# Performance work log

Hardware: AMD Instinct MI355X
Metric: run time of the kernel (lower is better)

Reference implementation:

```python
import jax, jax.numpy as jnp
import numpy as np

B, T, D_IN = 8192, 12, 64   # trajectories, traj length (== max_length), input dim
HID, ENC, R = 512, 128, 64  # encoder hidden, encoded_dim, MPS rank
OUT = 1


def _uniform(key, shape, bound):
    return jax.random.uniform(key, shape, jnp.float32, -bound, bound)


def setup_inputs() -> dict:
    key = jax.random.key(0)
    ks = jax.random.split(key, 8)
    x = jax.random.normal(ks[0], (B, T, D_IN), jnp.float32)
    # encoder Linear params (Kaiming-uniform-like scale)
    W1 = _uniform(ks[1], (HID, D_IN), 1.0 / np.sqrt(D_IN))
    b1 = _uniform(ks[2], (HID,), 1.0 / np.sqrt(D_IN))
    W2 = _uniform(ks[3], (ENC, HID), 1.0 / np.sqrt(HID))
    b2 = _uniform(ks[4], (ENC,), 1.0 / np.sqrt(HID))
    # MPS cores with if_rescale_weights bound = 1/sqrt(prod(dims))
    H_first = _uniform(ks[5], (1, ENC, R), 1.0 / np.sqrt(1 * ENC * R))
    H_mid = _uniform(ks[6], (T - 2, R, ENC, R), 1.0 / np.sqrt(R * ENC * R))
    H_last = _uniform(ks[7], (R, ENC, OUT), 1.0 / np.sqrt(R * ENC * OUT))
    return {"x": x, "W1": W1, "b1": b1, "W2": W2, "b2": b2,
            "H_first": H_first, "H_mid": H_mid, "H_last": H_last}


def reference(x, W1, b1, W2, b2, H_first, H_mid, H_last):
    Bn, Tn, _ = x.shape
    # two-layer encoder MLP with ReLU after each layer
    h = jax.nn.relu(jnp.einsum('btd,hd->bth', x, W1) + b1)
    enc = jax.nn.relu(jnp.einsum('bth,eh->bte', h, W2) + b2)  # [B, T, ENC]
    # contract each timestep's encoding with its core along the physical dim
    v = jnp.einsum('be,oer->br', enc[:, 0], H_first)              # [B, R] (dim0==1 squeezed)
    M = jnp.einsum('bte,tper->btpr', enc[:, 1:Tn - 1], H_mid)     # [B, T-2, R, R]
    # sequential chain product (vector-matrix, associative scan structure)
    for t in range(Tn - 2):
        v = jnp.einsum('bp,bpr->br', v, M[:, t])
    last = jnp.einsum('be,per->bpr', enc[:, -1], H_last)          # [B, R, OUT]
    out = jnp.einsum('bp,bpo->bo', v, last)                       # [B, OUT]
    return out.squeeze(-1)                                        # [B] (output_dim == 1)
```

## Files before the change

### kernel.cpp

```cpp
#include <hip/hip_runtime.h>
#include <hip/hip_fp16.h>


#define B_ALL 8192
#define TT    12
#define B_T   32
#define NBLK  256

typedef short bfrag __attribute__((ext_vector_type(8)));
typedef _Float16 hfrag __attribute__((ext_vector_type(8)));
typedef float ffrag __attribute__((ext_vector_type(16)));

#define O_ENC   0ULL
#define O_HMH   25165824ULL
#define O_HML   35651584ULL
#define O_W1F   46137344ULL
#define O_W2F   46202880ULL

__device__ __forceinline__ unsigned short bf16_rne(float f) {
    unsigned int u = __builtin_bit_cast(unsigned int, f);
    unsigned int r = (u + 0x7fffu + ((u >> 16) & 1u)) >> 16;
    return (unsigned short)r;
}
__device__ __forceinline__ float bf16_f32(unsigned short h) {
    unsigned int u = ((unsigned int)h) << 16;
    return __builtin_bit_cast(float, u);
}

__global__ __launch_bounds__(256)
void prep_kernel(const float* __restrict__ W1, const float* __restrict__ W2,
                 const float* __restrict__ Hm,
                 __half* __restrict__ w1f, __half* __restrict__ w2f,
                 unsigned short* __restrict__ Hh, unsigned short* __restrict__ Hl)
{
    const long long N_W1 = 32768, N_W2 = 65536, N_H = 10LL * 128 * 4096;
    const long long total = N_W1 + N_W2 + N_H;
    const long long stride = (long long)gridDim.x * blockDim.x;
    for (long long idx = (long long)blockIdx.x * blockDim.x + threadIdx.x;
         idx < total; idx += stride) {
        if (idx < N_W1) {
            const int w = (int)idx;
            const int jn = w >> 11, ks = (w >> 9) & 3, half = (w >> 8) & 1;
            const int jl = (w >> 3) & 31, jj = w & 7;
            const int j = jn * 32 + jl, d = ks * 16 + half * 8 + jj;
            w1f[w] = __float2half(W1[j * 64 + d]);
        } else if (idx < N_W1 + N_W2) {
            const int w = (int)(idx - N_W1);
            const int en = w >> 14, ks2g = (w >> 9) & 31, half = (w >> 8) & 1;
            const int el = (w >> 3) & 31, jj = w & 7;
            const int e = en * 32 + el, j = ks2g * 16 + half * 8 + jj;
            w2f[w] = __float2half(W2[e * 512 + j]);
        } else {
            const long long q = idx - N_W1 - N_W2;
            const int t = (int)(q / 524288);
            const int rem = (int)(q % 524288);
            const int e = rem >> 12;
            const int f = rem & 4095;
            const int mf = f >> 11, s = (f >> 9) & 3, half = (f >> 8) & 1;
            const int l = (f >> 3) & 31, j = f & 7;
            const int p = s * 16 + half * 8 + j;
            const int r = mf * 32 + l;
            const float val = Hm[(((long long)t * 64 + p) * 128 + e) * 64 + r];
            const unsigned short hi = bf16_rne(val);
            const unsigned short lo = bf16_rne(val - bf16_f32(hi));
            Hh[q] = hi;
            Hl[q] = lo;
        }
    }
}

__global__ __launch_bounds__(256)
void enc_kernel(const float* __restrict__ x,
                const float* __restrict__ b1, const float* __restrict__ b2,
                const __half* __restrict__ w1f, const __half* __restrict__ w2f,
                __half* __restrict__ encH)
{
    __shared__ __align__(16) unsigned char smem[17408];
    float* x_s  = (float*)smem;
    __half* h_s = (__half*)smem;

    const int tid   = threadIdx.x;
    const int wv    = tid >> 6;
    const int lane  = tid & 63;
    const int l32   = lane & 31;
    const int half  = lane >> 5;
    const int msub  = wv >> 1;
    const int nhalf = wv & 1;
    const int m0    = blockIdx.x * 64;

    #pragma unroll
    for (int i = 0; i < 4; ++i) {
        const int f4 = i * 256 + tid;
        const int r = f4 >> 4, c4 = (f4 & 15) * 4;
        *(float4*)&x_s[r * 68 + c4] =
            *(const float4*)&x[(long long)(m0 + r) * 64 + c4];
    }
    __syncthreads();

    hfrag xa[4];
    #pragma unroll
    for (int ks = 0; ks < 4; ++ks) {
        const float* src = &x_s[(msub * 32 + l32) * 68 + ks * 16 + half * 8];
        const float4 a = *(const float4*)src;
        const float4 b = *(const float4*)(src + 4);
        hfrag v;
        v[0] = (_Float16)a.x; v[1] = (_Float16)a.y;
        v[2] = (_Float16)a.z; v[3] = (_Float16)a.w;
        v[4] = (_Float16)b.x; v[5] = (_Float16)b.y;
        v[6] = (_Float16)b.z; v[7] = (_Float16)b.w;
        xa[ks] = v;
    }
    __syncthreads();

    ffrag c2[2];
    c2[0] = 0.0f; c2[1] = 0.0f;

    for (int chunk = 0; chunk < 4; ++chunk) {
        ffrag c1[2];
        float b1j[2];
        #pragma unroll
        for (int nf = 0; nf < 2; ++nf) {
            const int jn = chunk * 4 + nhalf * 2 + nf;
            b1j[nf] = b1[jn * 32 + l32];
            ffrag acc = 0.0f;
            #pragma unroll
            for (int ks = 0; ks < 4; ++ks) {
                const hfrag bh = *(const hfrag*)(w1f + (jn * 4 + ks) * 512
                                                 + half * 256 + l32 * 8);
                acc = __builtin_amdgcn_mfma_f32_32x32x16_f16(xa[ks], bh, acc, 0, 0, 0);
            }
            c1[nf] = acc;
        }
        __syncthreads();
        #pragma unroll
        for (int nf = 0; nf < 2; ++nf) {
            #pragma unroll
            for (int i2 = 0; i2 < 16; ++i2) {
                const int m_row = (i2 & 3) + 8 * (i2 >> 2) + 4 * half;
                const float v = fmaxf(c1[nf][i2] + b1j[nf], 0.0f);
                h_s[(msub * 32 + m_row) * 136 + nhalf * 64 + nf * 32 + l32] =
                    __float2half(v);
            }
        }
        __syncthreads();
        #pragma unroll
        for (int ks2 = 0; ks2 < 8; ++ks2) {
            const hfrag a = *(const hfrag*)&h_s[(msub * 32 + l32) * 136
                                                + ks2 * 16 + half * 8];
            const int ks2g = chunk * 8 + ks2;
            #pragma unroll
            for (int ef = 0; ef < 2; ++ef) {
                const int en = nhalf * 2 + ef;
                const hfrag b = *(const hfrag*)(w2f + (en * 32 + ks2g) * 512
                                                + half * 256 + l32 * 8);
                c2[ef] = __builtin_amdgcn_mfma_f32_32x32x16_f16(a, b, c2[ef], 0, 0, 0);
            }
        }
    }

    #pragma unroll
    for (int ef = 0; ef < 2; ++ef) {
        const int e = nhalf * 64 + ef * 32 + l32;
        const float b2e = b2[e];
        #pragma unroll
        for (int i2 = 0; i2 < 16; ++i2) {
            const int m_row = (i2 & 3) + 8 * (i2 >> 2) + 4 * half;
            const int m_g = m0 + msub * 32 + m_row;
            encH[(long long)m_g * 128 + e] =
                __float2half(fmaxf(c2[ef][i2] + b2e, 0.0f));
        }
    }
}

__global__ __launch_bounds__(512, 1)
void chain_all(const unsigned short* __restrict__ HmH,
               const unsigned short* __restrict__ HmL,
               const __half* __restrict__ encH,
               const float* __restrict__ Hf,
               const float* __restrict__ HL,
               float* __restrict__ out)
{
    __shared__ __align__(16) unsigned char smem[60480];
    float* vsum  = (float*)smem;
    float* enc_s = (float*)(smem + 8448);
    float* scr   = (float*)(smem + 25344);
    float* hl_s  = (float*)(smem + 25344);
    float* red   = (float*)(smem + 58368);

    const int tid  = threadIdx.x;
    const int b0   = blockIdx.x * B_T;
    const int lane = tid & 63;
    const int wv   = tid >> 6;
    const int l32  = lane & 31;
    const int half = lane >> 5;
    const int eq   = wv >> 1;
    const int rh   = wv & 1;

    const int sbL = tid >> 4;
    const int seo = (tid & 15) * 8;
    #define STAGE_ENC(T)                                                      \
    {                                                                         \
        const __half* er = encH + ((size_t)(b0 + sbL) * 12 + (T)) * 128 + seo;\
        uint4 u = *(const uint4*)er;                                          \
        const __half* hp = (const __half*)&u;                                 \
        _Pragma("unroll")                                                     \
        for (int j = 0; j < 8; ++j)                                           \
            enc_s[(seo + j) * 33 + sbL] = __half2float(hp[j]);                \
    }

    {
        STAGE_ENC(0);
        __syncthreads();
        const int bI = tid & 31, pg = tid >> 5;
        const int p0 = pg * 4;
        float a0 = 0, a1 = 0, a2 = 0, a3 = 0;
        for (int e = 0; e < 128; ++e) {
            const float ev = enc_s[e * 33 + bI];
            const float4 h = *(const float4*)&Hf[e * 64 + p0];
            a0 += ev * h.x; a1 += ev * h.y; a2 += ev * h.z; a3 += ev * h.w;
        }
        vsum[(p0 + 0) * 33 + bI] = a0;
        vsum[(p0 + 1) * 33 + bI] = a1;
        vsum[(p0 + 2) * 33 + bI] = a2;
        vsum[(p0 + 3) * 33 + bI] = a3;
        __syncthreads();
    }

    const unsigned short* Hsh = HmH;
    const unsigned short* Hsl = HmL;
    const int lanoff = rh * 2048 + half * 256 + l32 * 8;

    #pragma unroll 1
    for (int t = 1; t <= 10; ++t) {
        STAGE_ENC(t);

        bfrag vbh[4], vbl[4];
        #pragma unroll
        for (int s = 0; s < 4; ++s) {
            const int p0 = s * 16 + half * 8;
            bfrag hb, lb;
            #pragma unroll
            for (int j = 0; j < 8; ++j) {
                const float f = vsum[(p0 + j) * 33 + l32];
                const unsigned short hi = bf16_rne(f);
                const unsigned short lo = bf16_rne(f - bf16_f32(hi));
                hb[j] = (short)hi;
                lb[j] = (short)lo;
            }
            vbh[s] = hb;
            vbl[s] = lb;
        }
        __syncthreads();

        const unsigned short* hp = Hsh + (size_t)(eq * 32) * 4096 + lanoff;
        const unsigned short* lp = Hsl + (size_t)(eq * 32) * 4096 + lanoff;
        bfrag cah[4], cal[4];
        #pragma unroll
        for (int s = 0; s < 4; ++s) {
            cah[s] = *(const bfrag*)(hp + s * 512);
            cal[s] = *(const bfrag*)(lp + s * 512);
        }
        ffrag z = 0.0f;
        ffrag vn = 0.0f;
        #pragma unroll 2
        for (int e = 0; e < 32; ++e) {
            hp += 4096; lp += 4096;
            bfrag nah[4], nal[4];
            #pragma unroll
            for (int s = 0; s < 4; ++s) {
                nah[s] = *(const bfrag*)(hp + s * 512);
                nal[s] = *(const bfrag*)(lp + s * 512);
            }
            const float ev = enc_s[(eq * 32 + e) * 33 + l32];
            ffrag w = z;
            #pragma unroll
            for (int s = 0; s < 4; ++s) {
                w = __builtin_amdgcn_mfma_f32_32x32x16_bf16(cah[s], vbh[s], w, 0, 0, 0);
                w = __builtin_amdgcn_mfma_f32_32x32x16_bf16(cah[s], vbl[s], w, 0, 0, 0);
                w = __builtin_amdgcn_mfma_f32_32x32x16_bf16(cal[s], vbh[s], w, 0, 0, 0);
            }
            vn += w * ev;
            #pragma unroll
            for (int s = 0; s < 4; ++s) { cah[s] = nah[s]; cal[s] = nal[s]; }
        }
        __syncthreads();

        float4* sc4 = (float4*)scr;
        if (eq != 0) {
            const int slot = (eq - 1) * 2 + rh;
            #pragma unroll
            for (int q = 0; q < 4; ++q) {
                float4 f4 = {vn[q * 4 + 0], vn[q * 4 + 1],
                             vn[q * 4 + 2], vn[q * 4 + 3]};
                sc4[(slot * 4 + q) * 66 + lane] = f4;
            }
        }
        __syncthreads();
        if (eq == 0) {
            #pragma unroll
            for (int g = 1; g < 4; ++g) {
                const int slot = (g - 1) * 2 + rh;
                #pragma unroll
                for (int q = 0; q < 4; ++q) {
                    const float4 f4 = sc4[(slot * 4 + q) * 66 + lane];
                    vn[q * 4 + 0] += f4.x; vn[q * 4 + 1] += f4.y;
                    vn[q * 4 + 2] += f4.z; vn[q * 4 + 3] += f4.w;
                }
            }
            #pragma unroll
            for (int i = 0; i < 16; ++i) {
                const int r = rh * 32 + (i & 3) + 8 * (i >> 2) + 4 * half;
                vsum[r * 33 + l32] = vn[i];
            }
        }
        __syncthreads();

        Hsh += 524288;
        Hsl += 524288;
    }

    {
        STAGE_ENC(11);
        #pragma unroll
        for (int i = 0; i < 16; ++i) {
            const int idx = i * 512 + tid;
            hl_s[(idx >> 7) * 129 + (idx & 127)] = HL[idx];
        }
        __syncthreads();
        const int bI = tid & 31, pg = tid >> 5;
        const int p0 = pg * 4;
        float s = 0.0f;
        #pragma unroll
        for (int i = 0; i < 4; ++i) {
            float L = 0.0f;
            #pragma unroll 16
            for (int e = 0; e < 128; ++e)
                L += enc_s[e * 33 + bI] * hl_s[(p0 + i) * 129 + e];
            s += vsum[(p0 + i) * 33 + bI] * L;
        }
        red[pg * 33 + bI] = s;
        __syncthreads();
        if (tid < 32) {
            float acc = 0.0f;
            #pragma unroll
            for (int g = 0; g < 16; ++g)
                acc += red[g * 33 + tid];
            out[b0 + tid] = acc;
        }
    }
    #undef STAGE_ENC
}

extern "C" void kernel_launch(void* const* d_in, const int* in_sizes, int n_in,
                              void* d_out, int out_size, void* d_ws, size_t ws_size,
                              hipStream_t stream) {
    const float* x  = (const float*)d_in[0];
    const float* W1 = (const float*)d_in[1];
    const float* b1 = (const float*)d_in[2];
    const float* W2 = (const float*)d_in[3];
    const float* b2 = (const float*)d_in[4];
    const float* Hf = (const float*)d_in[5];
    const float* Hm = (const float*)d_in[6];
    const float* HL = (const float*)d_in[7];
    float* out = (float*)d_out;
    (void)in_sizes; (void)n_in; (void)out_size; (void)ws_size;

    char* ws = (char*)d_ws;
    __half* encH        = (__half*)(ws + O_ENC);
    unsigned short* HmH = (unsigned short*)(ws + O_HMH);
    unsigned short* HmL = (unsigned short*)(ws + O_HML);
    __half* w1f         = (__half*)(ws + O_W1F);
    __half* w2f         = (__half*)(ws + O_W2F);

    prep_kernel<<<dim3(5216), dim3(256), 0, stream>>>(W1, W2, Hm, w1f, w2f, HmH, HmL);
    enc_kernel<<<dim3(1536), dim3(256), 0, stream>>>(x, b1, b2, w1f, w2f, encH);
    chain_all<<<dim3(NBLK), dim3(512), 0, stream>>>(HmH, HmL, encH, Hf, HL, out);
}
```

Baseline: 402.9 us.

## Deepen H-core prefetch to distance two and rotate e-order per block group

The MPS core fragments (hi/lo bf16) are now prefetched two iterations ahead using a three-slot register ring. The first two loads are issued before the encoder staging and the v split, so their latency overlaps that work. The e-loop is fully unrolled, and each group of 8 blocks starts at a different rotated offset, so concurrent blocks read different parts of H_mid and contend less on the same cache lines. This raises register pressure: 24 fragments held live, plus full unrolling. That could lower occupancy or cause spills.

```diff
diff --git a/kernel.cpp b/kernel.cpp
--- a/kernel.cpp
+++ b/kernel.cpp
@@ -195,17 +195,18 @@
     const int half = lane >> 5;
     const int eq   = wv >> 1;
     const int rh   = wv & 1;
+    const int rot  = (int)((blockIdx.x >> 3) & 31);
 
     const int sbL = tid >> 4;
     const int seo = (tid & 15) * 8;
     #define STAGE_ENC(T)                                                      \
     {                                                                         \
-        const __half* er = encH + ((size_t)(b0 + sbL) * 12 + (T)) * 128 + seo;\
-        uint4 u = *(const uint4*)er;                                          \
-        const __half* hp = (const __half*)&u;                                 \
+        const __half* er_ = encH + ((size_t)(b0 + sbL) * 12 + (T)) * 128 + seo;\
+        uint4 u = *(const uint4*)er_;                                         \
+        const __half* hp_ = (const __half*)&u;                                \
         _Pragma("unroll")                                                     \
         for (int j = 0; j < 8; ++j)                                           \
-            enc_s[(seo + j) * 33 + sbL] = __half2float(hp[j]);                \
+            enc_s[(seo + j) * 33 + sbL] = __half2float(hp_[j]);               \
     }
 
     {
@@ -232,6 +233,20 @@
 
     #pragma unroll 1
     for (int t = 1; t <= 10; ++t) {
+        const unsigned short* Hq = Hsh + (size_t)(eq * 32) * 4096 + lanoff;
+        const unsigned short* Lq = Hsl + (size_t)(eq * 32) * 4096 + lanoff;
+
+        bfrag pah[3][4], pal[3][4];
+        #pragma unroll
+        for (int i = 0; i < 2; ++i) {
+            const int er = (i + rot) & 31;
+            #pragma unroll
+            for (int s = 0; s < 4; ++s) {
+                pah[i][s] = *(const bfrag*)(Hq + (size_t)er * 4096 + s * 512);
+                pal[i][s] = *(const bfrag*)(Lq + (size_t)er * 4096 + s * 512);
+            }
+        }
+
         STAGE_ENC(t);
 
         bfrag vbh[4], vbl[4];
@@ -252,36 +267,30 @@
         }
         __syncthreads();
 
-        const unsigned short* hp = Hsh + (size_t)(eq * 32) * 4096 + lanoff;
-        const unsigned short* lp = Hsl + (size_t)(eq * 32) * 4096 + lanoff;
-        bfrag cah[4], cal[4];
-        #pragma unroll
-        for (int s = 0; s < 4; ++s) {
-            cah[s] = *(const bfrag*)(hp + s * 512);
-            cal[s] = *(const bfrag*)(lp + s * 512);
-        }
         ffrag z = 0.0f;
         ffrag vn = 0.0f;
-        #pragma unroll 2
+        #pragma unroll
         for (int e = 0; e < 32; ++e) {
-            hp += 4096; lp += 4096;
-            bfrag nah[4], nal[4];
+            if (e < 30) {
+                const int erp = (e + 2 + rot) & 31;
+                const int sl = (e + 2) % 3;
+                #pragma unroll
+                for (int s = 0; s < 4; ++s) {
+                    pah[sl][s] = *(const bfrag*)(Hq + (size_t)erp * 4096 + s * 512);
+                    pal[sl][s] = *(const bfrag*)(Lq + (size_t)erp * 4096 + s * 512);
+                }
+            }
+            const int er = (e + rot) & 31;
+            const float ev = enc_s[(eq * 32 + er) * 33 + l32];
+            const int cs = e % 3;
+            ffrag w = z;
             #pragma unroll
             for (int s = 0; s < 4; ++s) {
-                nah[s] = *(const bfrag*)(hp + s * 512);
-                nal[s] = *(const bfrag*)(lp + s * 512);
-            }
-            const float ev = enc_s[(eq * 32 + e) * 33 + l32];
-            ffrag w = z;
-            #pragma unroll
-            for (int s = 0; s < 4; ++s) {
-                w = __builtin_amdgcn_mfma_f32_32x32x16_bf16(cah[s], vbh[s], w, 0, 0, 0);
-                w = __builtin_amdgcn_mfma_f32_32x32x16_bf16(cah[s], vbl[s], w, 0, 0, 0);
-                w = __builtin_amdgcn_mfma_f32_32x32x16_bf16(cal[s], vbh[s], w, 0, 0, 0);
+                w = __builtin_amdgcn_mfma_f32_32x32x16_bf16(pah[cs][s], vbh[s], w, 0, 0, 0);
+                w = __builtin_amdgcn_mfma_f32_32x32x16_bf16(pah[cs][s], vbl[s], w, 0, 0, 0);
+                w = __builtin_amdgcn_mfma_f32_32x32x16_bf16(pal[cs][s], vbh[s], w, 0, 0, 0);
             }
             vn += w * ev;
-            #pragma unroll
-            for (int s = 0; s < 4; ++s) { cah[s] = nah[s]; cal[s] = nal[s]; }
         }
         __syncthreads();
 
```

New measurement: 415.0 us. +3.0%, slower.

## Pair chain blocks across output-rank halves with global-memory exchange; tile prep transpose

Applied to the files above, without the earlier changes.

The chain kernel now pairs blocks so that each pair handles 64 trajectories, with each block computing half of the 64 output ranks. This doubles the batch width per MFMA operand and halves the weight traffic per block. After every step the partner blocks swap their halves of the state vector through a global buffer, using agent-scope atomics and a spin-wait flag. The prep kernel is also restructured so each block transposes one (t,e) slice of H through shared memory and writes it with vector stores, instead of doing strided scalar writes. This adds inter-block synchronisation, which assumes both blocks of a pair are co-resident and carries a deadlock risk.

```diff
diff --git a/kernel.cpp b/kernel.cpp
--- a/kernel.cpp
+++ b/kernel.cpp
@@ -4,8 +4,6 @@
 
 #define B_ALL 8192
 #define TT    12
-#define B_T   32
-#define NBLK  256
 
 typedef short bfrag __attribute__((ext_vector_type(8)));
 typedef _Float16 hfrag __attribute__((ext_vector_type(8)));
@@ -16,6 +14,7 @@
 #define O_HML   35651584ULL
 #define O_W1F   46137344ULL
 #define O_W2F   46202880ULL
+#define O_VBUF  46333952ULL
 
 __device__ __forceinline__ unsigned short bf16_rne(float f) {
     unsigned int u = __builtin_bit_cast(unsigned int, f);
@@ -25,6 +24,16 @@
 __device__ __forceinline__ float bf16_f32(unsigned short h) {
     unsigned int u = ((unsigned int)h) << 16;
     return __builtin_bit_cast(float, u);
+}
+
+__device__ __forceinline__ void st_f1_sc1(float* p, float v) {
+    __hip_atomic_store(p, v, __ATOMIC_RELAXED, __HIP_MEMORY_SCOPE_AGENT);
+}
+__device__ __forceinline__ float2 ld_f2_sc1(const float* p) {
+    unsigned long long u = __hip_atomic_load((unsigned long long*)(size_t)p,
+                                             __ATOMIC_RELAXED,
+                                             __HIP_MEMORY_SCOPE_AGENT);
+    return __builtin_bit_cast(float2, u);
 }
 
 __global__ __launch_bounds__(256)
@@ -33,38 +42,54 @@
                  __half* __restrict__ w1f, __half* __restrict__ w2f,
                  unsigned short* __restrict__ Hh, unsigned short* __restrict__ Hl)
 {
-    const long long N_W1 = 32768, N_W2 = 65536, N_H = 10LL * 128 * 4096;
-    const long long total = N_W1 + N_W2 + N_H;
-    const long long stride = (long long)gridDim.x * blockDim.x;
-    for (long long idx = (long long)blockIdx.x * blockDim.x + threadIdx.x;
-         idx < total; idx += stride) {
-        if (idx < N_W1) {
-            const int w = (int)idx;
-            const int jn = w >> 11, ks = (w >> 9) & 3, half = (w >> 8) & 1;
-            const int jl = (w >> 3) & 31, jj = w & 7;
-            const int j = jn * 32 + jl, d = ks * 16 + half * 8 + jj;
-            w1f[w] = __float2half(W1[j * 64 + d]);
-        } else if (idx < N_W1 + N_W2) {
-            const int w = (int)(idx - N_W1);
-            const int en = w >> 14, ks2g = (w >> 9) & 31, half = (w >> 8) & 1;
-            const int el = (w >> 3) & 31, jj = w & 7;
-            const int e = en * 32 + el, j = ks2g * 16 + half * 8 + jj;
-            w2f[w] = __float2half(W2[e * 512 + j]);
-        } else {
-            const long long q = idx - N_W1 - N_W2;
-            const int t = (int)(q / 524288);
-            const int rem = (int)(q % 524288);
-            const int e = rem >> 12;
-            const int f = rem & 4095;
-            const int mf = f >> 11, s = (f >> 9) & 3, half = (f >> 8) & 1;
-            const int l = (f >> 3) & 31, j = f & 7;
-            const int p = s * 16 + half * 8 + j;
-            const int r = mf * 32 + l;
-            const float val = Hm[(((long long)t * 64 + p) * 128 + e) * 64 + r];
-            const unsigned short hi = bf16_rne(val);
-            const unsigned short lo = bf16_rne(val - bf16_f32(hi));
-            Hh[q] = hi;
-            Hl[q] = lo;
+    const int tid = threadIdx.x;
+    const int bid = blockIdx.x;
+    if (bid < 1280) {
+        __shared__ unsigned short hs[4096], ls[4096];
+        const int t = bid >> 7, e = bid & 127;
+        const float* src = Hm + ((size_t)t * 64 * 128 + e) * 64;
+        const int p  = tid >> 2;
+        const int rc = (tid & 3) * 16;
+        const int fp = (p >> 4) * 512 + ((p >> 3) & 1) * 256 + (p & 7);
+        #pragma unroll
+        for (int k4 = 0; k4 < 4; ++k4) {
+            const int r0 = rc + k4 * 4;
+            const float4 v4 = *(const float4*)&src[(size_t)p * 8192 + r0];
+            const float vv[4] = {v4.x, v4.y, v4.z, v4.w};
+            #pragma unroll
+            for (int k = 0; k < 4; ++k) {
+                const int r = r0 + k;
+                const int f = (r >> 5) * 2048 + (r & 31) * 8 + fp;
+                const float val = vv[k];
+                const unsigned short hi = bf16_rne(val);
+                const unsigned short lo = bf16_rne(val - bf16_f32(hi));
+                hs[f] = hi;
+                ls[f] = lo;
+            }
+        }
+        __syncthreads();
+        const size_t q0 = (size_t)t * 524288 + (size_t)e * 4096 + tid * 16;
+        *(uint4*)&Hh[q0]     = *(const uint4*)&hs[tid * 16];
+        *(uint4*)&Hh[q0 + 8] = *(const uint4*)&hs[tid * 16 + 8];
+        *(uint4*)&Hl[q0]     = *(const uint4*)&ls[tid * 16];
+        *(uint4*)&Hl[q0 + 8] = *(const uint4*)&ls[tid * 16 + 8];
+    } else {
+        const int wb = bid - 1280;
+        const long long N_W1 = 32768, N_W2 = 65536;
+        for (long long idx = wb * 256 + tid; idx < N_W1 + N_W2; idx += 8 * 256) {
+            if (idx < N_W1) {
+                const int w = (int)idx;
+                const int jn = w >> 11, ks = (w >> 9) & 3, half = (w >> 8) & 1;
+                const int jl = (w >> 3) & 31, jj = w & 7;
+                const int j = jn * 32 + jl, d = ks * 16 + half * 8 + jj;
+                w1f[w] = __float2half(W1[j * 64 + d]);
+            } else {
+                const int w = (int)(idx - N_W1);
+                const int en = w >> 14, ks2g = (w >> 9) & 31, half = (w >> 8) & 1;
+                const int el = (w >> 3) & 31, jj = w & 7;
+                const int e = en * 32 + el, j = ks2g * 16 + half * 8 + jj;
+                w2f[w] = __float2half(W2[e * 512 + j]);
+            }
         }
     }
 }
@@ -172,83 +197,100 @@
     }
 }
 
+__device__ unsigned int g_flag[256 * 32];
+
 __global__ __launch_bounds__(512, 1)
 void chain_all(const unsigned short* __restrict__ HmH,
                const unsigned short* __restrict__ HmL,
                const __half* __restrict__ encH,
                const float* __restrict__ Hf,
                const float* __restrict__ HL,
+               float* vbuf,
                float* __restrict__ out)
 {
-    __shared__ __align__(16) unsigned char smem[60480];
+    __shared__ __align__(16) unsigned char smem[52800];
     float* vsum  = (float*)smem;
-    float* enc_s = (float*)(smem + 8448);
-    float* scr   = (float*)(smem + 25344);
-    float* hl_s  = (float*)(smem + 25344);
-    float* red   = (float*)(smem + 58368);
+    float* enc_s = (float*)(smem + 16896);
+    float* red   = (float*)(smem + 50688);
 
     const int tid  = threadIdx.x;
-    const int b0   = blockIdx.x * B_T;
+    const int bid  = blockIdx.x;
+    const int pid  = bid >> 1;
+    const int rr   = bid & 1;
+    const int b0   = pid * 64;
     const int lane = tid & 63;
     const int wv   = tid >> 6;
     const int l32  = lane & 31;
     const int half = lane >> 5;
     const int eq   = wv >> 1;
-    const int rh   = wv & 1;
-
-    const int sbL = tid >> 4;
-    const int seo = (tid & 15) * 8;
-    #define STAGE_ENC(T)                                                      \
-    {                                                                         \
-        const __half* er = encH + ((size_t)(b0 + sbL) * 12 + (T)) * 128 + seo;\
-        uint4 u = *(const uint4*)er;                                          \
-        const __half* hp = (const __half*)&u;                                 \
-        _Pragma("unroll")                                                     \
-        for (int j = 0; j < 8; ++j)                                           \
-            enc_s[(seo + j) * 33 + sbL] = __half2float(hp[j]);                \
+    const int bh   = wv & 1;
+    const int bcol = bh * 32 + l32;
+
+    unsigned int fbase = 0;
+    if (tid == 0)
+        fbase = __hip_atomic_load(&g_flag[bid * 32], __ATOMIC_RELAXED,
+                                  __HIP_MEMORY_SCOPE_AGENT);
+
+    const int sbL = tid >> 3;
+    const int seo = (tid & 7) * 16;
+    #define STAGE_ENC(T)                                                        \
+    {                                                                           \
+        const __half* er_ = encH + ((size_t)(b0 + sbL) * 12 + (T)) * 128 + seo; \
+        uint4 u0_ = *(const uint4*)er_;                                         \
+        uint4 u1_ = *(const uint4*)(er_ + 8);                                   \
+        const __half* hp_ = (const __half*)&u0_;                                \
+        const __half* hq_ = (const __half*)&u1_;                                \
+        _Pragma("unroll")                                                       \
+        for (int j = 0; j < 8; ++j)                                             \
+            enc_s[(seo + j) * 66 + sbL] = __half2float(hp_[j]);                 \
+        _Pragma("unroll")                                                       \
+        for (int j = 0; j < 8; ++j)                                             \
+            enc_s[(seo + 8 + j) * 66 + sbL] = __half2float(hq_[j]);             \
     }
 
     {
         STAGE_ENC(0);
         __syncthreads();
-        const int bI = tid & 31, pg = tid >> 5;
-        const int p0 = pg * 4;
-        float a0 = 0, a1 = 0, a2 = 0, a3 = 0;
+        const int pg = tid >> 6, bI = tid & 63;
+        float acc[8] = {0, 0, 0, 0, 0, 0, 0, 0};
         for (int e = 0; e < 128; ++e) {
-            const float ev = enc_s[e * 33 + bI];
-            const float4 h = *(const float4*)&Hf[e * 64 + p0];
-            a0 += ev * h.x; a1 += ev * h.y; a2 += ev * h.z; a3 += ev * h.w;
-        }
-        vsum[(p0 + 0) * 33 + bI] = a0;
-        vsum[(p0 + 1) * 33 + bI] = a1;
-        vsum[(p0 + 2) * 33 + bI] = a2;
-        vsum[(p0 + 3) * 33 + bI] = a3;
+            const float ev = enc_s[e * 66 + bI];
+            const float4 h0 = *(const float4*)&Hf[e * 64 + pg * 8];
+            const float4 h1 = *(const float4*)&Hf[e * 64 + pg * 8 + 4];
+            acc[0] += ev * h0.x; acc[1] += ev * h0.y;
+            acc[2] += ev * h0.z; acc[3] += ev * h0.w;
+            acc[4] += ev * h1.x; acc[5] += ev * h1.y;
+            acc[6] += ev * h1.z; acc[7] += ev * h1.w;
+        }
+        #pragma unroll
+        for (int i = 0; i < 8; ++i)
+            vsum[(pg * 8 + i) * 66 + bI] = acc[i];
         __syncthreads();
     }
 
     const unsigned short* Hsh = HmH;
     const unsigned short* Hsl = HmL;
-    const int lanoff = rh * 2048 + half * 256 + l32 * 8;
+    const int lanoff = rr * 2048 + half * 256 + l32 * 8;
 
     #pragma unroll 1
     for (int t = 1; t <= 10; ++t) {
         STAGE_ENC(t);
 
-        bfrag vbh[4], vbl[4];
+        bfrag vbh_[4], vbl_[4];
         #pragma unroll
         for (int s = 0; s < 4; ++s) {
             const int p0 = s * 16 + half * 8;
             bfrag hb, lb;
             #pragma unroll
             for (int j = 0; j < 8; ++j) {
-                const float f = vsum[(p0 + j) * 33 + l32];
+                const float f = vsum[(p0 + j) * 66 + bcol];
                 const unsigned short hi = bf16_rne(f);
                 const unsigned short lo = bf16_rne(f - bf16_f32(hi));
                 hb[j] = (short)hi;
                 lb[j] = (short)lo;
             }
-            vbh[s] = hb;
-            vbl[s] = lb;
+            vbh_[s] = hb;
+            vbl_[s] = lb;
         }
         __syncthreads();
 
@@ -271,13 +313,13 @@
                 nah[s] = *(const bfrag*)(hp + s * 512);
                 nal[s] = *(const bfrag*)(lp + s * 512);
             }
-            const float ev = enc_s[(eq * 32 + e) * 33 + l32];
+            const float ev = enc_s[(eq * 32 + e) * 66 + bcol];
             ffrag w = z;
             #pragma unroll
             for (int s = 0; s < 4; ++s) {
-                w = __builtin_amdgcn_mfma_f32_32x32x16_bf16(cah[s], vbh[s], w, 0, 0, 0);
-                w = __builtin_amdgcn_mfma_f32_32x32x16_bf16(cah[s], vbl[s], w, 0, 0, 0);
-                w = __builtin_amdgcn_mfma_f32_32x32x16_bf16(cal[s], vbh[s], w, 0, 0, 0);
+                w = __builtin_amdgcn_mfma_f32_32x32x16_bf16(cah[s], vbh_[s], w, 0, 0, 0);
+                w = __builtin_amdgcn_mfma_f32_32x32x16_bf16(cah[s], vbl_[s], w, 0, 0, 0);
+                w = __builtin_amdgcn_mfma_f32_32x32x16_bf16(cal[s], vbh_[s], w, 0, 0, 0);
             }
             vn += w * ev;
             #pragma unroll
@@ -285,9 +327,9 @@
         }
         __syncthreads();
 
-        float4* sc4 = (float4*)scr;
+        float4* sc4 = (float4*)enc_s;
         if (eq != 0) {
-            const int slot = (eq - 1) * 2 + rh;
+            const int slot = (eq - 1) * 2 + bh;
             #pragma unroll
             for (int q = 0; q < 4; ++q) {
                 float4 f4 = {vn[q * 4 + 0], vn[q * 4 + 1],
@@ -299,7 +341,7 @@
         if (eq == 0) {
             #pragma unroll
             for (int g = 1; g < 4; ++g) {
-                const int slot = (g - 1) * 2 + rh;
+                const int slot = (g - 1) * 2 + bh;
                 #pragma unroll
                 for (int q = 0; q < 4; ++q) {
                     const float4 f4 = sc4[(slot * 4 + q) * 66 + lane];
@@ -307,11 +349,33 @@
                     vn[q * 4 + 2] += f4.z; vn[q * 4 + 3] += f4.w;
                 }
             }
+            float* vb = vbuf + (((size_t)pid * 2 + (t & 1)) * 2 + rr) * 2048;
             #pragma unroll
             for (int i = 0; i < 16; ++i) {
-                const int r = rh * 32 + (i & 3) + 8 * (i >> 2) + 4 * half;
-                vsum[r * 33 + l32] = vn[i];
-            }
+                const int roffs = (i & 3) + 8 * (i >> 2) + 4 * half;
+                vsum[(rr * 32 + roffs) * 66 + bcol] = vn[i];
+                st_f1_sc1(&vb[roffs * 64 + bcol], vn[i]);
+            }
+        }
+        __syncthreads();
+
+        if (tid == 0) {
+            __hip_atomic_store(&g_flag[bid * 32], fbase + t, __ATOMIC_RELAXED,
+                               __HIP_MEMORY_SCOPE_AGENT);
+            while (__hip_atomic_load(&g_flag[(bid ^ 1) * 32], __ATOMIC_RELAXED,
+                                     __HIP_MEMORY_SCOPE_AGENT) < fbase + t)
+                __builtin_amdgcn_s_sleep(8);
+        }
+        __syncthreads();
+
+        {
+            const float* pb = vbuf + (((size_t)pid * 2 + (t & 1)) * 2 + (rr ^ 1)) * 2048;
+            const int i4 = tid * 4;
+            const int r_l = i4 >> 6, bc = i4 & 63;
+            const float2 u0 = ld_f2_sc1(pb + i4);
+            const float2 u1 = ld_f2_sc1(pb + i4 + 2);
+            float* dst = &vsum[((rr ^ 1) * 32 + r_l) * 66 + bc];
+            dst[0] = u0.x; dst[1] = u0.y; dst[2] = u1.x; dst[3] = u1.y;
         }
         __syncthreads();
 
@@ -321,30 +385,25 @@
 
     {
         STAGE_ENC(11);
-        #pragma unroll
-        for (int i = 0; i < 16; ++i) {
-            const int idx = i * 512 + tid;
-            hl_s[(idx >> 7) * 129 + (idx & 127)] = HL[idx];
-        }
-        __syncthreads();
-        const int bI = tid & 31, pg = tid >> 5;
-        const int p0 = pg * 4;
+        __syncthreads();
+        const int pg = tid >> 6, bI = tid & 63;
         float s = 0.0f;
         #pragma unroll
-        for (int i = 0; i < 4; ++i) {
+        for (int i = 0; i < 8; ++i) {
+            const int p = pg * 8 + i;
             float L = 0.0f;
             #pragma unroll 16
             for (int e = 0; e < 128; ++e)
-                L += enc_s[e * 33 + bI] * hl_s[(p0 + i) * 129 + e];
-            s += vsum[(p0 + i) * 33 + bI] * L;
-        }
-        red[pg * 33 + bI] = s;
-        __syncthreads();
-        if (tid < 32) {
+                L += enc_s[e * 66 + bI] * HL[p * 128 + e];
+            s += vsum[p * 66 + bI] * L;
+        }
+        red[pg * 66 + bI] = s;
+        __syncthreads();
+        if (rr == 0 && tid < 64) {
             float acc = 0.0f;
             #pragma unroll
-            for (int g = 0; g < 16; ++g)
-                acc += red[g * 33 + tid];
+            for (int g = 0; g < 8; ++g)
+                acc += red[g * 66 + tid];
             out[b0 + tid] = acc;
         }
     }
@@ -371,8 +430,9 @@
     unsigned short* HmL = (unsigned short*)(ws + O_HML);
     __half* w1f         = (__half*)(ws + O_W1F);
     __half* w2f         = (__half*)(ws + O_W2F);
-
-    prep_kernel<<<dim3(5216), dim3(256), 0, stream>>>(W1, W2, Hm, w1f, w2f, HmH, HmL);
+    float* vbuf         = (float*)(ws + O_VBUF);
+
+    prep_kernel<<<dim3(1288), dim3(256), 0, stream>>>(W1, W2, Hm, w1f, w2f, HmH, HmL);
     enc_kernel<<<dim3(1536), dim3(256), 0, stream>>>(x, b1, b2, w1f, w2f, encH);
-    chain_all<<<dim3(NBLK), dim3(512), 0, stream>>>(HmH, HmL, encH, Hf, HL, out);
-}
+    chain_all<<<dim3(256), dim3(512), 0, stream>>>(HmH, HmL, encH, Hf, HL, vbuf, out);
+}
```

New measurement: 446.4 us. 1.11x slower.
